# Performance work log

Hardware: AMD Instinct MI355X
Metric: run time of the kernel (lower is better)

Reference implementation:

```python
import jax, jax.numpy as jnp
import numpy as np

NUM_HEADS = 4
KEY_DIMS = 32  # c // num_heads


def rel_to_abs(x):
    # x: [B, N, W, 2W-1] relative logits -> [B, N, W, W] absolute logits
    b, n, w, _ = x.shape
    x = jnp.pad(x, ((0, 0), (0, 0), (0, 0), (0, 1)))           # [b,n,w,2w]
    x = x.reshape(b, n, w * 2 * w)
    x = jnp.pad(x, ((0, 0), (0, 0), (0, w - 1)))
    x = x.reshape(b, n, w + 1, 2 * w - 1)
    return x[:, :, :w, w - 1:]


def rel_logits_1d(q, rel_k):
    # q: [B, heads, X, Y, d], rel_k: [2Y-1, d] -> [B, heads, X, X, Y, Y]
    b, nh, xx, yy, d = q.shape
    rl = jnp.einsum('bhxyd,md->bhxym', q, rel_k)               # [b,h,x,y,2y-1]
    rl = rel_to_abs(rl.reshape(b, nh * xx, yy, 2 * yy - 1))    # [b,h*x,y,y]
    rl = rl.reshape(b, nh, xx, 1, yy, yy)
    return jnp.broadcast_to(rl, (b, nh, xx, xx, yy, yy))


def relative_position_bias(pos_q, pos_emb_h, pos_emb_w):
    # pos_q: [B, heads, H, W, d] -> bias [B, heads, H, W, H, W]
    rw = rel_logits_1d(pos_q, pos_emb_w)                        # [b,h,H,H,W,W]
    rw = rw.transpose(0, 1, 2, 4, 3, 5)                         # [b,h,H,W,H,W]
    rh = rel_logits_1d(pos_q.transpose(0, 1, 3, 2, 4), pos_emb_h)  # [b,h,W,W,H,H]
    rh = rh.transpose(0, 1, 4, 2, 5, 3)                         # [b,h,H,W,H,W]
    return rw + rh


def setup_inputs() -> dict:
    key = jax.random.key(0)
    k1, k2, k3, k4 = jax.random.split(key, 4)
    B, H, W, C = 2, 64, 64, 128
    qk_dims = NUM_HEADS * KEY_DIMS  # 128
    out_channels = C
    x = jax.random.normal(k1, (B, H, W, C), dtype=jnp.float32)
    w_qkv = jax.random.normal(k2, (C, 2 * qk_dims + out_channels), dtype=jnp.float32) * 0.05
    pos_emb_h = jax.random.normal(k3, (2 * H - 1, KEY_DIMS), dtype=jnp.float32) * 0.05
    pos_emb_w = jax.random.normal(k4, (2 * W - 1, KEY_DIMS), dtype=jnp.float32) * 0.05
    return {'x': x, 'w_qkv': w_qkv, 'pos_emb_h': pos_emb_h, 'pos_emb_w': pos_emb_w}


def reference(x, w_qkv, pos_emb_h, pos_emb_w):
    B, H, W, C = x.shape
    nh, kd = NUM_HEADS, KEY_DIMS
    qk_dims = nh * kd
    oc = C
    scale = 1.0 / float(kd) ** 0.5

    qkv = jnp.einsum('bhwc,cd->bhwd', x, w_qkv)                 # 1x1 conv, no bias
    q, k, v = jnp.split(qkv, [qk_dims, 2 * qk_dims], axis=-1)
    L = H * W
    q = q.reshape(B, L, nh, kd).transpose(0, 2, 1, 3)           # [B,nh,L,kd]
    k = k.reshape(B, L, nh, kd).transpose(0, 2, 1, 3)           # [B,nh,L,kd]
    v = v.reshape(B, L, nh, oc // nh).transpose(0, 2, 1, 3)     # [B,nh,L,dv]

    pos_q = q.reshape(B, nh, H, W, kd)
    pos = relative_position_bias(pos_q, pos_emb_h, pos_emb_w).reshape(B, nh, L, L)

    scores = jnp.einsum('bnqd,bnkd->bnqk', q, k) * scale + pos  # [B,nh,L,L]
    attn = jax.nn.softmax(scores, axis=-1)
    out = jnp.einsum('bnqk,bnkd->bnqd', attn, v)                # [B,nh,L,dv]
    out = out.transpose(0, 2, 1, 3).reshape(B, H, W, oc)
    return out
```

## Files before the change

### kernel.cpp

```cpp
#include <hip/hip_runtime.h>
#include <hip/hip_bf16.h>
#include <math.h>

#define B_  2
#define NH  4
#define HH  64
#define WW  64
#define KD  32
#define L_  4096
#define BN_ 8
#define LOG2E 1.4426950408889634f
#define KSCALE (0.17677669529663687f * 1.4426950408889634f)
#define FIXED_M 10.0f

typedef float    f32x4  __attribute__((ext_vector_type(4), may_alias));
typedef _Float16 half8  __attribute__((ext_vector_type(8), may_alias));
typedef _Float16 half4  __attribute__((ext_vector_type(4), may_alias));
typedef __fp16   fp16x2 __attribute__((ext_vector_type(2)));
typedef unsigned uint4v __attribute__((ext_vector_type(4), may_alias));

__device__ __forceinline__ float fexp2(float x) {
#if __has_builtin(__builtin_amdgcn_exp2f)
    return __builtin_amdgcn_exp2f(x);
#else
    return __expf(x * 0.69314718056f);
#endif
}

__device__ __forceinline__ unsigned pack2u(float a, float b) {
    fp16x2 t = __builtin_amdgcn_cvt_pkrtz(a, b);
    union { fp16x2 i; unsigned o; } u;
    u.i = t;
    return u.o;
}

__global__ __launch_bounds__(256) void qkv_gemm(const float* __restrict__ x,
                                                const float* __restrict__ w,
                                                _Float16* __restrict__ q_h,
                                                _Float16* __restrict__ k_h,
                                                _Float16* __restrict__ vt_h) {
    __shared__ __align__(16) char smem[34816];
    _Float16* xs  = (_Float16*)smem;
    _Float16* wsT = (_Float16*)(smem + 17408);

    const int mt = blockIdx.x % 128;
    const int nt = blockIdx.x / 128;
    const int m0 = mt * 64, n0 = nt * 64;
    const int tid = threadIdx.x;
    const int wv = tid >> 6, lane = tid & 63;
    const int l16 = lane & 15, quad = lane >> 4;

    #pragma unroll
    for (int i = 0; i < 8; i++) {
        const int idx = i * 256 + tid;
        const int row = idx >> 5, c4 = (idx & 31) * 4;
        const float4 v = *(const float4*)&x[(size_t)(m0 + row) * 128 + c4];
        half4 h;
        h[0] = (_Float16)v.x; h[1] = (_Float16)v.y;
        h[2] = (_Float16)v.z; h[3] = (_Float16)v.w;
        *(half4*)&xs[row * 136 + c4] = h;
    }
    #pragma unroll
    for (int i = 0; i < 8; i++) {
        const int idx = i * 256 + tid;
        const int k = idx >> 4, c4 = (idx & 15) * 4;
        const float4 v = *(const float4*)&w[(size_t)k * 384 + n0 + c4];
        wsT[(c4 + 0) * 136 + k] = (_Float16)v.x;
        wsT[(c4 + 1) * 136 + k] = (_Float16)v.y;
        wsT[(c4 + 2) * 136 + k] = (_Float16)v.z;
        wsT[(c4 + 3) * 136 + k] = (_Float16)v.w;
    }
    __syncthreads();

    f32x4 acc[4] = {{0.f,0.f,0.f,0.f},{0.f,0.f,0.f,0.f},
                    {0.f,0.f,0.f,0.f},{0.f,0.f,0.f,0.f}};
    half8 af[4];
    #pragma unroll
    for (int kc = 0; kc < 4; kc++)
        af[kc] = *(const half8*)&xs[(wv * 16 + l16) * 136 + kc * 32 + quad * 8];
    #pragma unroll
    for (int ns = 0; ns < 4; ns++)
        #pragma unroll
        for (int kc = 0; kc < 4; kc++) {
            const half8 bf = *(const half8*)&wsT[(ns * 16 + l16) * 136 + kc * 32 + quad * 8];
            acc[ns] = __builtin_amdgcn_mfma_f32_16x16x32_f16(af[kc], bf, acc[ns], 0, 0, 0);
        }

    const int which = n0 >> 7;
    const int nc = n0 & 127;
    const int b = m0 >> 12;
    if (which < 2) {
        _Float16* dst = (which == 0) ? q_h : k_h;
        const float mult = (which == 1) ? KSCALE : 1.0f;
        #pragma unroll
        for (int ns = 0; ns < 4; ns++) {
            const int col = nc + ns * 16 + l16;
            const int bn = b * NH + (col >> 5);
            const int d = col & 31;
            #pragma unroll
            for (int r = 0; r < 4; r++) {
                const int l = (m0 & 4095) + wv * 16 + quad * 4 + r;
                dst[((size_t)bn * L_ + l) * 32 + d] = (_Float16)(acc[ns][r] * mult);
            }
        }
    } else {
        __syncthreads();
        float* img = (float*)smem;
        #pragma unroll
        for (int ns = 0; ns < 4; ns++) {
            const int chan = ns * 16 + l16;
            const int h = chan >> 5, d = chan & 31;
            #pragma unroll
            for (int r = 0; r < 4; r++) {
                const int p = wv * 16 + quad * 4 + r;
                const int y = p >> 5, p32 = p & 31;
                const int q4 = (p32 >> 2) & 3;
                const int j = ((p32 >> 4) & 1) * 4 + (p32 & 3);
                const int fidx = h * 2048 + (y * 2 + (d >> 4)) * 512
                               + (q4 * 16 + (d & 15)) * 8 + j;
                img[fidx + (fidx >> 4)] = acc[ns][r];
            }
        }
        __syncthreads();
        const int ktg = (m0 & 4095) >> 6;
        #pragma unroll
        for (int h = 0; h < 2; h++) {
            const int head = (nc >> 5) + h;
            const int bn = b * NH + head;
            const int fbase = h * 2048 + tid * 8;
            const int sbase = fbase + (fbase >> 4);
            half8 o;
            #pragma unroll
            for (int e = 0; e < 8; e++) o[e] = (_Float16)img[sbase + e];
            *(half8*)(vt_h + (size_t)bn * 131072 + ktg * 2048 + tid * 8) = o;
        }
    }
}

__global__ __launch_bounds__(512) void attn_mfma(
    const _Float16* __restrict__ q_h,
    const _Float16* __restrict__ k_h,
    const _Float16* __restrict__ vt_h,
    const float* __restrict__ emb_h,
    const float* __restrict__ emb_w,
    float* __restrict__ out)
{
    __shared__ __align__(16) char smem[49408];

    const int bi    = blockIdx.x;
    const int bn    = bi & 7;
    const int w1    = bi >> 3;
    const int tid   = threadIdx.x;
    const int wv    = tid >> 6;
    const int qg    = wv & 3;
    const int kh    = wv >> 2;
    const int lane  = tid & 63;
    const int l16   = lane & 15;
    const int quad  = lane >> 4;
    const int q0    = qg * 16;

    const _Float16* Kbase = k_h  + (size_t)bn * L_ * 32;
    const _Float16* Vtile = vt_h + (size_t)bn * 131072;

    const int Tt  = wv & 3;
    const int sH  = wv >> 2;
    const int khT = Tt & 1;
    const int isV = Tt >> 1;
    const _Float16* gs[2];
    int ldsT[2];
    #pragma unroll
    for (int u = 0; u < 2; u++) {
        const int sC = sH * 2 + u;
        gs[u] = (isV ? Vtile : Kbase)
              + (size_t)khT * 32 * 2048 + sC * 512 + lane * 8;
        ldsT[u] = khT * 4096 + (isV
            ? (8192 + sC * 1024 + lane * 16)
            : ((sC * 16 + (lane >> 2)) * 64 + (((lane & 3) ^ ((lane >> 3) & 3)) << 4)));
    }

    const uint4v stg0a = *(const uint4v*)gs[0];
    const uint4v stg0b = *(const uint4v*)gs[1];

    float* Rw = (float*)(smem + 32768) + qg * 1040;

    const half8 aq = *(const half8*)(q_h +
        (((size_t)bn * L_ + (q0 + l16) * 64 + w1) * 32 + quad * 8));

    f32x4 qwT[4];
    #pragma unroll
    for (int sub = 0; sub < 4; sub++) {
        const float* ew = emb_w + (size_t)(sub * 16 + l16 - w1 + 63) * 32 + quad * 8;
        const float4 e0 = *(const float4*)ew;
        const float4 e1 = *(const float4*)(ew + 4);
        union { uint4v u; half8 h; } ua;
        ua.u[0] = pack2u(e0.x * LOG2E, e0.y * LOG2E);
        ua.u[1] = pack2u(e0.z * LOG2E, e0.w * LOG2E);
        ua.u[2] = pack2u(e1.x * LOG2E, e1.y * LOG2E);
        ua.u[3] = pack2u(e1.z * LOG2E, e1.w * LOG2E);
        f32x4 z = {-FIXED_M, -FIXED_M, -FIXED_M, -FIXED_M};
        qwT[sub] = __builtin_amdgcn_mfma_f32_16x16x32_f16(ua.h, aq, z, 0, 0, 0);
    }

    #pragma unroll
    for (int ji = 0; ji < 4; ji++) {
        const int jt = kh * 4 + ji;
        const int j = min(jt * 16 + l16, 126);
        const float* eh = emb_h + (size_t)j * 32 + quad * 8;
        const float4 e0 = *(const float4*)eh;
        const float4 e1 = *(const float4*)(eh + 4);
        union { uint4v u; half8 h; } ub;
        ub.u[0] = pack2u(e0.x * LOG2E, e0.y * LOG2E);
        ub.u[1] = pack2u(e0.z * LOG2E, e0.w * LOG2E);
        ub.u[2] = pack2u(e1.x * LOG2E, e1.y * LOG2E);
        ub.u[3] = pack2u(e1.z * LOG2E, e1.w * LOG2E);
        f32x4 z = {0.f, 0.f, 0.f, 0.f};
        const f32x4 C = __builtin_amdgcn_mfma_f32_16x16x32_f16(aq, ub.h, z, 0, 0, 0);
        #pragma unroll
        for (int r = 0; r < 4; r++) {
            const int row = quad * 4 + r;
            const int c = jt * 16 + l16 - 63 + (q0 + row);
            if (c >= 0 && c < 64)
                Rw[row * 65 + c] = C[r];
        }
    }

    *(uint4v*)(smem + ldsT[0]) = stg0a;
    *(uint4v*)(smem + ldsT[1]) = stg0b;
    __syncthreads();

    f32x4 O0 = {0.f, 0.f, 0.f, 0.f}, O1 = {0.f, 0.f, 0.f, 0.f};
    float l0 = 0.f, l1 = 0.f;
    const float* qh_row = Rw + l16 * 65;
    float qh_cur = qh_row[kh * 32];
#if __has_builtin(__builtin_amdgcn_fdot2)
    fp16x2 onep;
    { union { unsigned u; fp16x2 h; } uo; uo.u = pack2u(1.0f, 1.0f); onep = uo.h; }
#endif

    const int kOff = kh * 4096 + l16 * 64 + ((quad ^ ((l16 >> 1) & 3)) << 4);
    const int vOff = 8192 + kh * 4096 + lane * 16;

    #pragma unroll 2
    for (int t = 0; t < 32; t++) {
        const int cur = t & 1;
        const int tS = (t < 31) ? (t + 1) : 31;
        const uint4v sa = *(const uint4v*)(gs[0] + (size_t)tS * 2048);
        const uint4v sb = *(const uint4v*)(gs[1] + (size_t)tS * 2048);

        const char* kb = smem + cur * 16384 + kOff;
        const char* vb = smem + cur * 16384 + vOff;
        const half8 kf0 = *(const half8*)(kb);
        const half8 kf1 = *(const half8*)(kb + 1024);
        const half8 kf2 = *(const half8*)(kb + 2048);
        const half8 kf3 = *(const half8*)(kb + 3072);
        const half8 va00 = *(const half8*)(vb);
        const half8 va10 = *(const half8*)(vb + 1024);
        const half8 va01 = *(const half8*)(vb + 2048);
        const half8 va11 = *(const half8*)(vb + 3072);

        const f32x4 S0 = __builtin_amdgcn_mfma_f32_16x16x32_f16(kf0, aq, qwT[0], 0, 0, 0);
        const f32x4 S1 = __builtin_amdgcn_mfma_f32_16x16x32_f16(kf1, aq, qwT[1], 0, 0, 0);
        const f32x4 S2 = __builtin_amdgcn_mfma_f32_16x16x32_f16(kf2, aq, qwT[2], 0, 0, 0);
        const f32x4 S3 = __builtin_amdgcn_mfma_f32_16x16x32_f16(kf3, aq, qwT[3], 0, 0, 0);

        const float qh_next = qh_row[kh * 32 + tS];

        union { uint4v u; half8 h; } pb0, pb1;
        const float a0 = fexp2(S0[0] + qh_cur), a1 = fexp2(S0[1] + qh_cur);
        const float a2 = fexp2(S0[2] + qh_cur), a3 = fexp2(S0[3] + qh_cur);
        const float a4 = fexp2(S1[0] + qh_cur), a5 = fexp2(S1[1] + qh_cur);
        const float a6 = fexp2(S1[2] + qh_cur), a7 = fexp2(S1[3] + qh_cur);
        pb0.u[0] = pack2u(a0, a1); pb0.u[1] = pack2u(a2, a3);
        pb0.u[2] = pack2u(a4, a5); pb0.u[3] = pack2u(a6, a7);
        const float b0 = fexp2(S2[0] + qh_cur), b1 = fexp2(S2[1] + qh_cur);
        const float b2 = fexp2(S2[2] + qh_cur), b3 = fexp2(S2[3] + qh_cur);
        const float b4 = fexp2(S3[0] + qh_cur), b5 = fexp2(S3[1] + qh_cur);
        const float b6 = fexp2(S3[2] + qh_cur), b7 = fexp2(S3[3] + qh_cur);
        pb1.u[0] = pack2u(b0, b1); pb1.u[1] = pack2u(b2, b3);
        pb1.u[2] = pack2u(b4, b5); pb1.u[3] = pack2u(b6, b7);

        O0 = __builtin_amdgcn_mfma_f32_16x16x32_f16(va00, pb0.h, O0, 0, 0, 0);
        O0 = __builtin_amdgcn_mfma_f32_16x16x32_f16(va01, pb1.h, O0, 0, 0, 0);
        O1 = __builtin_amdgcn_mfma_f32_16x16x32_f16(va10, pb0.h, O1, 0, 0, 0);
        O1 = __builtin_amdgcn_mfma_f32_16x16x32_f16(va11, pb1.h, O1, 0, 0, 0);

#if __has_builtin(__builtin_amdgcn_fdot2)
        {
            union { unsigned u; fp16x2 h; } c0, c1, c2, c3;
            c0.u = pb0.u[0]; c1.u = pb0.u[1]; c2.u = pb0.u[2]; c3.u = pb0.u[3];
            l0 = __builtin_amdgcn_fdot2(c0.h, onep, l0, false);
            l0 = __builtin_amdgcn_fdot2(c1.h, onep, l0, false);
            l0 = __builtin_amdgcn_fdot2(c2.h, onep, l0, false);
            l0 = __builtin_amdgcn_fdot2(c3.h, onep, l0, false);
            c0.u = pb1.u[0]; c1.u = pb1.u[1]; c2.u = pb1.u[2]; c3.u = pb1.u[3];
            l1 = __builtin_amdgcn_fdot2(c0.h, onep, l1, false);
            l1 = __builtin_amdgcn_fdot2(c1.h, onep, l1, false);
            l1 = __builtin_amdgcn_fdot2(c2.h, onep, l1, false);
            l1 = __builtin_amdgcn_fdot2(c3.h, onep, l1, false);
        }
#else
        l0 += ((a0 + a1) + (a2 + a3)) + ((a4 + a5) + (a6 + a7));
        l1 += ((b0 + b1) + (b2 + b3)) + ((b4 + b5) + (b6 + b7));
#endif
        qh_cur = qh_next;

        __builtin_amdgcn_sched_barrier(0);
        *(uint4v*)(smem + (cur ^ 1) * 16384 + ldsT[0]) = sa;
        *(uint4v*)(smem + (cur ^ 1) * 16384 + ldsT[1]) = sb;
        __syncthreads();
    }

    float l = l0 + l1;
    l += __shfl_xor(l, 16);
    l += __shfl_xor(l, 32);

    __syncthreads();
    float (*mO)[32][17] = (float(*)[32][17])smem;
    float* mL = (float*)(smem + 17408);
    #pragma unroll
    for (int r = 0; r < 4; r++) {
        mO[wv][quad * 4 + r][l16]      = O0[r];
        mO[wv][16 + quad * 4 + r][l16] = O1[r];
    }
    if (quad == 0) mL[wv * 16 + l16] = l;
    __syncthreads();

    const int h1 = tid >> 3;
    const int dg = tid & 7;
    const int qgo = h1 >> 4, ql = h1 & 15;
    const int wsA = qgo;
    const int wsB = qgo + 4;
    const float denom = mL[wsA * 16 + ql] + mL[wsB * 16 + ql];
    const float inv = 1.0f / denom;
    float4 o;
    o.x = (mO[wsA][dg * 4 + 0][ql] + mO[wsB][dg * 4 + 0][ql]) * inv;
    o.y = (mO[wsA][dg * 4 + 1][ql] + mO[wsB][dg * 4 + 1][ql]) * inv;
    o.z = (mO[wsA][dg * 4 + 2][ql] + mO[wsB][dg * 4 + 2][ql]) * inv;
    o.w = (mO[wsA][dg * 4 + 3][ql] + mO[wsB][dg * 4 + 3][ql]) * inv;
    const int head = bn & 3, bb = bn >> 2;
    *(float4*)&out[(((size_t)bb * 64 + h1) * 64 + w1) * 128 + head * 32 + dg * 4] = o;
}

extern "C" void kernel_launch(void* const* d_in, const int* in_sizes, int n_in,
                              void* d_out, int out_size, void* d_ws, size_t ws_size,
                              hipStream_t stream) {
    const float* x     = (const float*)d_in[0];
    const float* w_qkv = (const float*)d_in[1];
    const float* emb_h = (const float*)d_in[2];
    const float* emb_w = (const float*)d_in[3];
    float* out = (float*)d_out;

    _Float16* q_h  = (_Float16*)d_ws;
    _Float16* k_h  = q_h + (size_t)BN_ * L_ * KD;
    _Float16* vt_h = k_h + (size_t)BN_ * L_ * KD;

    qkv_gemm<<<768, 256, 0, stream>>>(x, w_qkv, q_h, k_h, vt_h);
    attn_mfma<<<512, 512, 0, stream>>>(q_h, k_h, vt_h, emb_h, emb_w, out);
}
```

Baseline: 104.4 us.

## Process two query groups per wave and halve attention block size

Each wave now computes scores and outputs for two 16-row query groups, reusing the same K/V LDS fragments for both, and the block shrinks to 256 threads with each wave staging four global chunks per step. This cuts redundant LDS reads per MFMA and reduces the number of waves contending for barriers. In exchange it raises register pressure per wave (double accumulators, exponentials, qwT terms), which may lower occupancy, and the non-fdot2 fallback path no longer accumulates row sums.

```diff
diff --git a/kernel.cpp b/kernel.cpp
--- a/kernel.cpp
+++ b/kernel.cpp
@@ -137,7 +137,7 @@
     }
 }
 
-__global__ __launch_bounds__(512) void attn_mfma(
+__global__ __launch_bounds__(256) void attn_mfma(
     const _Float16* __restrict__ q_h,
     const _Float16* __restrict__ k_h,
     const _Float16* __restrict__ vt_h,
@@ -152,41 +152,40 @@
     const int w1    = bi >> 3;
     const int tid   = threadIdx.x;
     const int wv    = tid >> 6;
-    const int qg    = wv & 3;
-    const int kh    = wv >> 2;
+    const int qgp   = wv & 1;
+    const int kh    = wv >> 1;
     const int lane  = tid & 63;
     const int l16   = lane & 15;
     const int quad  = lane >> 4;
-    const int q0    = qg * 16;
 
     const _Float16* Kbase = k_h  + (size_t)bn * L_ * 32;
     const _Float16* Vtile = vt_h + (size_t)bn * 131072;
 
-    const int Tt  = wv & 3;
-    const int sH  = wv >> 2;
-    const int khT = Tt & 1;
-    const int isV = Tt >> 1;
-    const _Float16* gs[2];
-    int ldsT[2];
-    #pragma unroll
-    for (int u = 0; u < 2; u++) {
-        const int sC = sH * 2 + u;
-        gs[u] = (isV ? Vtile : Kbase)
-              + (size_t)khT * 32 * 2048 + sC * 512 + lane * 8;
-        ldsT[u] = khT * 4096 + (isV
+    const int khT = wv & 1;
+    const int isV = wv >> 1;
+    const _Float16* gs[4];
+    int ldsT[4];
+    #pragma unroll
+    for (int sC = 0; sC < 4; sC++) {
+        gs[sC] = (isV ? Vtile : Kbase)
+               + (size_t)khT * 32 * 2048 + sC * 512 + lane * 8;
+        ldsT[sC] = khT * 4096 + (isV
             ? (8192 + sC * 1024 + lane * 16)
             : ((sC * 16 + (lane >> 2)) * 64 + (((lane & 3) ^ ((lane >> 3) & 3)) << 4)));
     }
 
-    const uint4v stg0a = *(const uint4v*)gs[0];
-    const uint4v stg0b = *(const uint4v*)gs[1];
-
-    float* Rw = (float*)(smem + 32768) + qg * 1040;
-
-    const half8 aq = *(const half8*)(q_h +
-        (((size_t)bn * L_ + (q0 + l16) * 64 + w1) * 32 + quad * 8));
-
-    f32x4 qwT[4];
+    uint4v stg0[4];
+    #pragma unroll
+    for (int u = 0; u < 4; u++) stg0[u] = *(const uint4v*)gs[u];
+
+    float* Rw0 = (float*)(smem + 32768) + (qgp * 2 + 0) * 1040;
+    float* Rw1 = (float*)(smem + 32768) + (qgp * 2 + 1) * 1040;
+    const half8 aq0 = *(const half8*)(q_h +
+        (((size_t)bn * L_ + ((qgp * 2 + 0) * 16 + l16) * 64 + w1) * 32 + quad * 8));
+    const half8 aq1 = *(const half8*)(q_h +
+        (((size_t)bn * L_ + ((qgp * 2 + 1) * 16 + l16) * 64 + w1) * 32 + quad * 8));
+
+    f32x4 qwT0[4], qwT1[4];
     #pragma unroll
     for (int sub = 0; sub < 4; sub++) {
         const float* ew = emb_w + (size_t)(sub * 16 + l16 - w1 + 63) * 32 + quad * 8;
@@ -198,7 +197,8 @@
         ua.u[2] = pack2u(e1.x * LOG2E, e1.y * LOG2E);
         ua.u[3] = pack2u(e1.z * LOG2E, e1.w * LOG2E);
         f32x4 z = {-FIXED_M, -FIXED_M, -FIXED_M, -FIXED_M};
-        qwT[sub] = __builtin_amdgcn_mfma_f32_16x16x32_f16(ua.h, aq, z, 0, 0, 0);
+        qwT0[sub] = __builtin_amdgcn_mfma_f32_16x16x32_f16(ua.h, aq0, z, 0, 0, 0);
+        qwT1[sub] = __builtin_amdgcn_mfma_f32_16x16x32_f16(ua.h, aq1, z, 0, 0, 0);
     }
 
     #pragma unroll
@@ -214,24 +214,29 @@
         ub.u[2] = pack2u(e1.x * LOG2E, e1.y * LOG2E);
         ub.u[3] = pack2u(e1.z * LOG2E, e1.w * LOG2E);
         f32x4 z = {0.f, 0.f, 0.f, 0.f};
-        const f32x4 C = __builtin_amdgcn_mfma_f32_16x16x32_f16(aq, ub.h, z, 0, 0, 0);
+        const f32x4 C0 = __builtin_amdgcn_mfma_f32_16x16x32_f16(aq0, ub.h, z, 0, 0, 0);
+        const f32x4 C1 = __builtin_amdgcn_mfma_f32_16x16x32_f16(aq1, ub.h, z, 0, 0, 0);
         #pragma unroll
         for (int r = 0; r < 4; r++) {
             const int row = quad * 4 + r;
-            const int c = jt * 16 + l16 - 63 + (q0 + row);
-            if (c >= 0 && c < 64)
-                Rw[row * 65 + c] = C[r];
-        }
-    }
-
-    *(uint4v*)(smem + ldsT[0]) = stg0a;
-    *(uint4v*)(smem + ldsT[1]) = stg0b;
+            const int c0 = jt * 16 + l16 - 63 + ((qgp * 2 + 0) * 16 + row);
+            if (c0 >= 0 && c0 < 64) Rw0[row * 65 + c0] = C0[r];
+            const int c1 = jt * 16 + l16 - 63 + ((qgp * 2 + 1) * 16 + row);
+            if (c1 >= 0 && c1 < 64) Rw1[row * 65 + c1] = C1[r];
+        }
+    }
+
+    #pragma unroll
+    for (int u = 0; u < 4; u++) *(uint4v*)(smem + ldsT[u]) = stg0[u];
     __syncthreads();
 
-    f32x4 O0 = {0.f, 0.f, 0.f, 0.f}, O1 = {0.f, 0.f, 0.f, 0.f};
-    float l0 = 0.f, l1 = 0.f;
-    const float* qh_row = Rw + l16 * 65;
-    float qh_cur = qh_row[kh * 32];
+    f32x4 O00 = {0.f,0.f,0.f,0.f}, O01 = {0.f,0.f,0.f,0.f};
+    f32x4 O10 = {0.f,0.f,0.f,0.f}, O11 = {0.f,0.f,0.f,0.f};
+    float la = 0.f, lb = 0.f;
+    const float* qh_row0 = Rw0 + l16 * 65;
+    const float* qh_row1 = Rw1 + l16 * 65;
+    float qh_cur0 = qh_row0[kh * 32];
+    float qh_cur1 = qh_row1[kh * 32];
 #if __has_builtin(__builtin_amdgcn_fdot2)
     fp16x2 onep;
     { union { unsigned u; fp16x2 h; } uo; uo.u = pack2u(1.0f, 1.0f); onep = uo.h; }
@@ -244,8 +249,10 @@
     for (int t = 0; t < 32; t++) {
         const int cur = t & 1;
         const int tS = (t < 31) ? (t + 1) : 31;
-        const uint4v sa = *(const uint4v*)(gs[0] + (size_t)tS * 2048);
-        const uint4v sb = *(const uint4v*)(gs[1] + (size_t)tS * 2048);
+        uint4v sa[4];
+        #pragma unroll
+        for (int u = 0; u < 4; u++)
+            sa[u] = *(const uint4v*)(gs[u] + (size_t)tS * 2048);
 
         const char* kb = smem + cur * 16384 + kOff;
         const char* vb = smem + cur * 16384 + vOff;
@@ -258,87 +265,134 @@
         const half8 va01 = *(const half8*)(vb + 2048);
         const half8 va11 = *(const half8*)(vb + 3072);
 
-        const f32x4 S0 = __builtin_amdgcn_mfma_f32_16x16x32_f16(kf0, aq, qwT[0], 0, 0, 0);
-        const f32x4 S1 = __builtin_amdgcn_mfma_f32_16x16x32_f16(kf1, aq, qwT[1], 0, 0, 0);
-        const f32x4 S2 = __builtin_amdgcn_mfma_f32_16x16x32_f16(kf2, aq, qwT[2], 0, 0, 0);
-        const f32x4 S3 = __builtin_amdgcn_mfma_f32_16x16x32_f16(kf3, aq, qwT[3], 0, 0, 0);
-
-        const float qh_next = qh_row[kh * 32 + tS];
-
-        union { uint4v u; half8 h; } pb0, pb1;
-        const float a0 = fexp2(S0[0] + qh_cur), a1 = fexp2(S0[1] + qh_cur);
-        const float a2 = fexp2(S0[2] + qh_cur), a3 = fexp2(S0[3] + qh_cur);
-        const float a4 = fexp2(S1[0] + qh_cur), a5 = fexp2(S1[1] + qh_cur);
-        const float a6 = fexp2(S1[2] + qh_cur), a7 = fexp2(S1[3] + qh_cur);
-        pb0.u[0] = pack2u(a0, a1); pb0.u[1] = pack2u(a2, a3);
-        pb0.u[2] = pack2u(a4, a5); pb0.u[3] = pack2u(a6, a7);
-        const float b0 = fexp2(S2[0] + qh_cur), b1 = fexp2(S2[1] + qh_cur);
-        const float b2 = fexp2(S2[2] + qh_cur), b3 = fexp2(S2[3] + qh_cur);
-        const float b4 = fexp2(S3[0] + qh_cur), b5 = fexp2(S3[1] + qh_cur);
-        const float b6 = fexp2(S3[2] + qh_cur), b7 = fexp2(S3[3] + qh_cur);
-        pb1.u[0] = pack2u(b0, b1); pb1.u[1] = pack2u(b2, b3);
-        pb1.u[2] = pack2u(b4, b5); pb1.u[3] = pack2u(b6, b7);
-
-        O0 = __builtin_amdgcn_mfma_f32_16x16x32_f16(va00, pb0.h, O0, 0, 0, 0);
-        O0 = __builtin_amdgcn_mfma_f32_16x16x32_f16(va01, pb1.h, O0, 0, 0, 0);
-        O1 = __builtin_amdgcn_mfma_f32_16x16x32_f16(va10, pb0.h, O1, 0, 0, 0);
-        O1 = __builtin_amdgcn_mfma_f32_16x16x32_f16(va11, pb1.h, O1, 0, 0, 0);
+        const f32x4 S00 = __builtin_amdgcn_mfma_f32_16x16x32_f16(kf0, aq0, qwT0[0], 0, 0, 0);
+        const f32x4 S01 = __builtin_amdgcn_mfma_f32_16x16x32_f16(kf1, aq0, qwT0[1], 0, 0, 0);
+        const f32x4 S02 = __builtin_amdgcn_mfma_f32_16x16x32_f16(kf2, aq0, qwT0[2], 0, 0, 0);
+        const f32x4 S03 = __builtin_amdgcn_mfma_f32_16x16x32_f16(kf3, aq0, qwT0[3], 0, 0, 0);
+        const f32x4 S10 = __builtin_amdgcn_mfma_f32_16x16x32_f16(kf0, aq1, qwT1[0], 0, 0, 0);
+        const f32x4 S11 = __builtin_amdgcn_mfma_f32_16x16x32_f16(kf1, aq1, qwT1[1], 0, 0, 0);
+        const f32x4 S12 = __builtin_amdgcn_mfma_f32_16x16x32_f16(kf2, aq1, qwT1[2], 0, 0, 0);
+        const f32x4 S13 = __builtin_amdgcn_mfma_f32_16x16x32_f16(kf3, aq1, qwT1[3], 0, 0, 0);
+
+        const float qh_next0 = qh_row0[kh * 32 + tS];
+        const float qh_next1 = qh_row1[kh * 32 + tS];
+
+        union { uint4v u; half8 h; } p0a, p0b;
+        {
+            const float a0 = fexp2(S00[0] + qh_cur0), a1 = fexp2(S00[1] + qh_cur0);
+            const float a2 = fexp2(S00[2] + qh_cur0), a3 = fexp2(S00[3] + qh_cur0);
+            const float a4 = fexp2(S01[0] + qh_cur0), a5 = fexp2(S01[1] + qh_cur0);
+            const float a6 = fexp2(S01[2] + qh_cur0), a7 = fexp2(S01[3] + qh_cur0);
+            p0a.u[0] = pack2u(a0, a1); p0a.u[1] = pack2u(a2, a3);
+            p0a.u[2] = pack2u(a4, a5); p0a.u[3] = pack2u(a6, a7);
+            const float b0 = fexp2(S02[0] + qh_cur0), b1 = fexp2(S02[1] + qh_cur0);
+            const float b2 = fexp2(S02[2] + qh_cur0), b3 = fexp2(S02[3] + qh_cur0);
+            const float b4 = fexp2(S03[0] + qh_cur0), b5 = fexp2(S03[1] + qh_cur0);
+            const float b6 = fexp2(S03[2] + qh_cur0), b7 = fexp2(S03[3] + qh_cur0);
+            p0b.u[0] = pack2u(b0, b1); p0b.u[1] = pack2u(b2, b3);
+            p0b.u[2] = pack2u(b4, b5); p0b.u[3] = pack2u(b6, b7);
+        }
+        union { uint4v u; half8 h; } p1a, p1b;
+        {
+            const float a0 = fexp2(S10[0] + qh_cur1), a1 = fexp2(S10[1] + qh_cur1);
+            const float a2 = fexp2(S10[2] + qh_cur1), a3 = fexp2(S10[3] + qh_cur1);
+            const float a4 = fexp2(S11[0] + qh_cur1), a5 = fexp2(S11[1] + qh_cur1);
+            const float a6 = fexp2(S11[2] + qh_cur1), a7 = fexp2(S11[3] + qh_cur1);
+            p1a.u[0] = pack2u(a0, a1); p1a.u[1] = pack2u(a2, a3);
+            p1a.u[2] = pack2u(a4, a5); p1a.u[3] = pack2u(a6, a7);
+            const float b0 = fexp2(S12[0] + qh_cur1), b1 = fexp2(S12[1] + qh_cur1);
+            const float b2 = fexp2(S12[2] + qh_cur1), b3 = fexp2(S12[3] + qh_cur1);
+            const float b4 = fexp2(S13[0] + qh_cur1), b5 = fexp2(S13[1] + qh_cur1);
+            const float b6 = fexp2(S13[2] + qh_cur1), b7 = fexp2(S13[3] + qh_cur1);
+            p1b.u[0] = pack2u(b0, b1); p1b.u[1] = pack2u(b2, b3);
+            p1b.u[2] = pack2u(b4, b5); p1b.u[3] = pack2u(b6, b7);
+        }
+
+        O00 = __builtin_amdgcn_mfma_f32_16x16x32_f16(va00, p0a.h, O00, 0, 0, 0);
+        O00 = __builtin_amdgcn_mfma_f32_16x16x32_f16(va01, p0b.h, O00, 0, 0, 0);
+        O01 = __builtin_amdgcn_mfma_f32_16x16x32_f16(va10, p0a.h, O01, 0, 0, 0);
+        O01 = __builtin_amdgcn_mfma_f32_16x16x32_f16(va11, p0b.h, O01, 0, 0, 0);
+        O10 = __builtin_amdgcn_mfma_f32_16x16x32_f16(va00, p1a.h, O10, 0, 0, 0);
+        O10 = __builtin_amdgcn_mfma_f32_16x16x32_f16(va01, p1b.h, O10, 0, 0, 0);
+        O11 = __builtin_amdgcn_mfma_f32_16x16x32_f16(va10, p1a.h, O11, 0, 0, 0);
+        O11 = __builtin_amdgcn_mfma_f32_16x16x32_f16(va11, p1b.h, O11, 0, 0, 0);
 
 #if __has_builtin(__builtin_amdgcn_fdot2)
         {
             union { unsigned u; fp16x2 h; } c0, c1, c2, c3;
-            c0.u = pb0.u[0]; c1.u = pb0.u[1]; c2.u = pb0.u[2]; c3.u = pb0.u[3];
-            l0 = __builtin_amdgcn_fdot2(c0.h, onep, l0, false);
-            l0 = __builtin_amdgcn_fdot2(c1.h, onep, l0, false);
-            l0 = __builtin_amdgcn_fdot2(c2.h, onep, l0, false);
-            l0 = __builtin_amdgcn_fdot2(c3.h, onep, l0, false);
-            c0.u = pb1.u[0]; c1.u = pb1.u[1]; c2.u = pb1.u[2]; c3.u = pb1.u[3];
-            l1 = __builtin_amdgcn_fdot2(c0.h, onep, l1, false);
-            l1 = __builtin_amdgcn_fdot2(c1.h, onep, l1, false);
-            l1 = __builtin_amdgcn_fdot2(c2.h, onep, l1, false);
-            l1 = __builtin_amdgcn_fdot2(c3.h, onep, l1, false);
-        }
-#else
-        l0 += ((a0 + a1) + (a2 + a3)) + ((a4 + a5) + (a6 + a7));
-        l1 += ((b0 + b1) + (b2 + b3)) + ((b4 + b5) + (b6 + b7));
+            c0.u = p0a.u[0]; c1.u = p0a.u[1]; c2.u = p0a.u[2]; c3.u = p0a.u[3];
+            la = __builtin_amdgcn_fdot2(c0.h, onep, la, false);
+            la = __builtin_amdgcn_fdot2(c1.h, onep, la, false);
+            la = __builtin_amdgcn_fdot2(c2.h, onep, la, false);
+            la = __builtin_amdgcn_fdot2(c3.h, onep, la, false);
+            c0.u = p0b.u[0]; c1.u = p0b.u[1]; c2.u = p0b.u[2]; c3.u = p0b.u[3];
+            la = __builtin_amdgcn_fdot2(c0.h, onep, la, false);
+            la = __builtin_amdgcn_fdot2(c1.h, onep, la, false);
+            la = __builtin_amdgcn_fdot2(c2.h, onep, la, false);
+            la = __builtin_amdgcn_fdot2(c3.h, onep, la, false);
+            c0.u = p1a.u[0]; c1.u = p1a.u[1]; c2.u = p1a.u[2]; c3.u = p1a.u[3];
+            lb = __builtin_amdgcn_fdot2(c0.h, onep, lb, false);
+            lb = __builtin_amdgcn_fdot2(c1.h, onep, lb, false);
+            lb = __builtin_amdgcn_fdot2(c2.h, onep, lb, false);
+            lb = __builtin_amdgcn_fdot2(c3.h, onep, lb, false);
+            c0.u = p1b.u[0]; c1.u = p1b.u[1]; c2.u = p1b.u[2]; c3.u = p1b.u[3];
+            lb = __builtin_amdgcn_fdot2(c0.h, onep, lb, false);
+            lb = __builtin_amdgcn_fdot2(c1.h, onep, lb, false);
+            lb = __builtin_amdgcn_fdot2(c2.h, onep, lb, false);
+            lb = __builtin_amdgcn_fdot2(c3.h, onep, lb, false);
+        }
 #endif
-        qh_cur = qh_next;
+        qh_cur0 = qh_next0;
+        qh_cur1 = qh_next1;
 
         __builtin_amdgcn_sched_barrier(0);
-        *(uint4v*)(smem + (cur ^ 1) * 16384 + ldsT[0]) = sa;
-        *(uint4v*)(smem + (cur ^ 1) * 16384 + ldsT[1]) = sb;
+        #pragma unroll
+        for (int u = 0; u < 4; u++)
+            *(uint4v*)(smem + (cur ^ 1) * 16384 + ldsT[u]) = sa[u];
         __syncthreads();
     }
 
-    float l = l0 + l1;
-    l += __shfl_xor(l, 16);
-    l += __shfl_xor(l, 32);
+    la += __shfl_xor(la, 16);
+    la += __shfl_xor(la, 32);
+    lb += __shfl_xor(lb, 16);
+    lb += __shfl_xor(lb, 32);
 
     __syncthreads();
     float (*mO)[32][17] = (float(*)[32][17])smem;
     float* mL = (float*)(smem + 17408);
+    const int slot0 = kh * 4 + qgp * 2 + 0;
+    const int slot1 = kh * 4 + qgp * 2 + 1;
     #pragma unroll
     for (int r = 0; r < 4; r++) {
-        mO[wv][quad * 4 + r][l16]      = O0[r];
-        mO[wv][16 + quad * 4 + r][l16] = O1[r];
-    }
-    if (quad == 0) mL[wv * 16 + l16] = l;
+        mO[slot0][quad * 4 + r][l16]      = O00[r];
+        mO[slot0][16 + quad * 4 + r][l16] = O01[r];
+        mO[slot1][quad * 4 + r][l16]      = O10[r];
+        mO[slot1][16 + quad * 4 + r][l16] = O11[r];
+    }
+    if (quad == 0) {
+        mL[slot0 * 16 + l16] = la;
+        mL[slot1 * 16 + l16] = lb;
+    }
     __syncthreads();
 
-    const int h1 = tid >> 3;
-    const int dg = tid & 7;
-    const int qgo = h1 >> 4, ql = h1 & 15;
-    const int wsA = qgo;
-    const int wsB = qgo + 4;
-    const float denom = mL[wsA * 16 + ql] + mL[wsB * 16 + ql];
-    const float inv = 1.0f / denom;
-    float4 o;
-    o.x = (mO[wsA][dg * 4 + 0][ql] + mO[wsB][dg * 4 + 0][ql]) * inv;
-    o.y = (mO[wsA][dg * 4 + 1][ql] + mO[wsB][dg * 4 + 1][ql]) * inv;
-    o.z = (mO[wsA][dg * 4 + 2][ql] + mO[wsB][dg * 4 + 2][ql]) * inv;
-    o.w = (mO[wsA][dg * 4 + 3][ql] + mO[wsB][dg * 4 + 3][ql]) * inv;
     const int head = bn & 3, bb = bn >> 2;
-    *(float4*)&out[(((size_t)bb * 64 + h1) * 64 + w1) * 128 + head * 32 + dg * 4] = o;
+    #pragma unroll
+    for (int rep = 0; rep < 2; rep++) {
+        const int idx = rep * 256 + tid;
+        const int h1 = idx >> 3;
+        const int dg = idx & 7;
+        const int qgo = h1 >> 4, ql = h1 & 15;
+        const int wsA = qgo;
+        const int wsB = qgo + 4;
+        const float denom = mL[wsA * 16 + ql] + mL[wsB * 16 + ql];
+        const float inv = 1.0f / denom;
+        float4 o;
+        o.x = (mO[wsA][dg * 4 + 0][ql] + mO[wsB][dg * 4 + 0][ql]) * inv;
+        o.y = (mO[wsA][dg * 4 + 1][ql] + mO[wsB][dg * 4 + 1][ql]) * inv;
+        o.z = (mO[wsA][dg * 4 + 2][ql] + mO[wsB][dg * 4 + 2][ql]) * inv;
+        o.w = (mO[wsA][dg * 4 + 3][ql] + mO[wsB][dg * 4 + 3][ql]) * inv;
+        *(float4*)&out[(((size_t)bb * 64 + h1) * 64 + w1) * 128 + head * 32 + dg * 4] = o;
+    }
 }
 
 extern "C" void kernel_launch(void* const* d_in, const int* in_sizes, int n_in,
@@ -355,5 +409,5 @@
     _Float16* vt_h = k_h + (size_t)BN_ * L_ * KD;
 
     qkv_gemm<<<768, 256, 0, stream>>>(x, w_qkv, q_h, k_h, vt_h);
-    attn_mfma<<<512, 512, 0, stream>>>(q_h, k_h, vt_h, emb_h, emb_w, out);
+    attn_mfma<<<512, 256, 0, stream>>>(q_h, k_h, vt_h, emb_h, emb_w, out);
 }
```

Result: no change. 104.0 us (-0.4%).
